# Optimization experiments

Measured on AMD Instinct MI355X. Metric: run time of the kernel, lower is better.

The kernel has to match this reference:

```python
import jax, jax.numpy as jnp
import numpy as np

N_NODES = 50000
N_EDGES = 800000
IN_F, EDGE_F, HID, HEADS, OUT_F = 128, 16, 32, 4, 128
NEG_SLOPE = 0.2


def edge_gat_layer(h, ef, src, dst, W, We, al, ar, ae, b, act):
    """One DGL-style EdgeGATConv layer.
    h: [N, Fin], ef: [E, Fe], W: [Fin, H*D], We: [Fe, H*D],
    al/ar/ae: [H, D], b: [H*D]. Returns [N, H*D].
    """
    N = h.shape[0]
    H, D = al.shape
    feat = (h @ W).reshape(N, H, D)                    # [N,H,D]
    fe = (ef @ We).reshape(-1, H, D)                   # [E,H,D]
    el = jnp.einsum('nhd,hd->nh', feat, al)            # [N,H]
    er = jnp.einsum('nhd,hd->nh', feat, ar)            # [N,H]
    ee = jnp.einsum('ehd,hd->eh', fe, ae)              # [E,H]
    e = jax.nn.leaky_relu(el[src] + er[dst] + ee, NEG_SLOPE)  # [E,H]
    # edge softmax over incoming edges of each dst node
    emax = jax.ops.segment_max(e, dst, num_segments=N)        # [N,H]
    ex = jnp.exp(e - emax[dst])                               # [E,H]
    esum = jax.ops.segment_sum(ex, dst, num_segments=N)       # [N,H]
    a = ex / esum[dst]                                        # [E,H]
    msg = feat[src] * a[:, :, None]                           # [E,H,D]
    rst = jax.ops.segment_sum(msg, dst, num_segments=N)       # [N,H,D]
    rst = rst + b.reshape(1, H, D)
    if act:
        rst = jax.nn.relu(rst)
    return rst.reshape(N, H * D)


def _glorot(k, shape):
    fan = shape[0]
    return jax.random.normal(k, shape, dtype=jnp.float32) / np.sqrt(fan)


def setup_inputs() -> dict:
    key = jax.random.key(0)
    ks = jax.random.split(key, 24)
    inp = {
        'h': jax.random.normal(ks[0], (N_NODES, IN_F), dtype=jnp.float32),
        'edge_feats': jax.random.normal(ks[1], (N_EDGES, EDGE_F), dtype=jnp.float32),
        'src': jax.random.randint(ks[2], (N_EDGES,), 0, N_NODES, dtype=jnp.int32),
        'dst': jax.random.randint(ks[3], (N_EDGES,), 0, N_NODES, dtype=jnp.int32),
    }
    # layer 0: IN_F -> HEADS*HID ; layer 1: HEADS*HID -> HEADS*HID ; layer 2: heads=1, OUT_F
    dims = [(IN_F, HEADS, HID), (HEADS * HID, HEADS, HID), (HEADS * HID, 1, OUT_F)]
    ki = 4
    for i, (fin, H, D) in enumerate(dims):
        inp[f'W{i}'] = _glorot(ks[ki], (fin, H * D)); ki += 1
        inp[f'We{i}'] = _glorot(ks[ki], (EDGE_F, H * D)); ki += 1
        inp[f'al{i}'] = _glorot(ks[ki], (H, D)); ki += 1
        inp[f'ar{i}'] = _glorot(ks[ki], (H, D)); ki += 1
        inp[f'ae{i}'] = _glorot(ks[ki], (H, D)); ki += 1
        inp[f'b{i}'] = jnp.zeros((H * D,), dtype=jnp.float32)
    return inp


def reference(h, edge_feats, src, dst,
              W0, We0, al0, ar0, ae0, b0,
              W1, We1, al1, ar1, ae1, b1,
              W2, We2, al2, ar2, ae2, b2):
    h = edge_gat_layer(h, edge_feats, src, dst, W0, We0, al0, ar0, ae0, b0, True)
    h = edge_gat_layer(h, edge_feats, src, dst, W1, We1, al1, ar1, ae1, b1, True)
    h = edge_gat_layer(h, edge_feats, src, dst, W2, We2, al2, ar2, ae2, b2, False)
    return h
```

## Files before the change

kernel.cpp:

```cpp
#include <hip/hip_runtime.h>
#include <hip/hip_fp16.h>
#include <cstdint>

#define NN 50000
#define NE 800000
static constexpr int HD = 128;
static constexpr int EF_DIM = 16;
static constexpr int SCAN_B = 256;
static constexpr int NPARTS = (NN + SCAN_B - 1) / SCAN_B;

typedef _Float16 f16x4 __attribute__((ext_vector_type(4)));
typedef float f32x4 __attribute__((ext_vector_type(4)));

struct RecP {
    int src;
    int e;
    f16x4 p0;
    f16x4 p1;
    _Float16 p2;
    _Float16 pad;
};
union Rec32 { RecP r; float4 v[2]; };

__global__ __launch_bounds__(256) void k_prep(const float* __restrict__ h,
        const float* __restrict__ We0, const float* __restrict__ ae0,
        const float* __restrict__ We1, const float* __restrict__ ae1,
        const float* __restrict__ We2, const float* __restrict__ ae2,
        const float* __restrict__ W0, const float* __restrict__ W1,
        const float* __restrict__ W2,
        int* __restrict__ cnt, float* __restrict__ M,
        _Float16* __restrict__ Wht, _Float16* __restrict__ Xh) {
    const int b = blockIdx.x, t = threadIdx.x;
    if (b < 196) {
        int i = b * 256 + t;
        if (i < NN) cnt[i] = 0;
        return;
    }
    if (b < 199) {
        int l = b - 196;
        const float* We = (l == 0) ? We0 : (l == 1) ? We1 : We2;
        const float* ae = (l == 0) ? ae0 : (l == 1) ? ae1 : ae2;
        int H = (l == 2) ? 1 : 4, D = (l == 2) ? 128 : 32;
        if (t < EF_DIM * H) {
            int f = t / H, hh = t % H;
            float s = 0.f;
            for (int d = 0; d < D; d++) s += We[f * HD + hh * D + d] * ae[hh * D + d];
            M[l * 64 + f * H + hh] = s;
        }
        return;
    }
    if (b < 391) {
        int i = (b - 199) * 256 + t;
        int l = i >> 14, rem = i & 16383;
        int n = rem >> 7, k = rem & 127;
        const float* W = (l == 0) ? W0 : (l == 1) ? W1 : W2;
        Wht[(size_t)l * 16384 + n * 128 + k] = (_Float16)W[k * 128 + n];
        return;
    }
    {
        int i = (b - 391) * 256 + t;
        if (i < NN * 32) {
            float4 v = ((const float4*)h)[i];
            f16x4 o = {(_Float16)v.x, (_Float16)v.y, (_Float16)v.z, (_Float16)v.w};
            ((f16x4*)Xh)[i] = o;
        }
    }
}


__global__ void k_pos(const int* __restrict__ dst, int* __restrict__ cnt,
                      int* __restrict__ pos_loc) {
    int e = blockIdx.x * blockDim.x + threadIdx.x;
    if (e < NE) pos_loc[e] = atomicAdd(&cnt[dst[e]], 1);
}

__global__ __launch_bounds__(SCAN_B) void k_part(const int* __restrict__ deg,
                                                 int* __restrict__ part) {
    __shared__ int s[SCAN_B];
    int t = threadIdx.x;
    int i = blockIdx.x * SCAN_B + t;
    s[t] = (i < NN) ? deg[i] : 0;
    __syncthreads();
    for (int off = SCAN_B / 2; off > 0; off >>= 1) {
        if (t < off) s[t] += s[t + off];
        __syncthreads();
    }
    if (t == 0) part[blockIdx.x] = s[0];
}

__global__ __launch_bounds__(SCAN_B) void k_scanpart(int* __restrict__ part) {
    __shared__ int s[SCAN_B];
    int t = threadIdx.x;
    int v = (t < NPARTS) ? part[t] : 0;
    s[t] = v;
    __syncthreads();
    for (int off = 1; off < SCAN_B; off <<= 1) {
        int u = (t >= off) ? s[t - off] : 0;
        __syncthreads();
        s[t] += u;
        __syncthreads();
    }
    if (t < NPARTS) part[t] = s[t] - v;
}

__global__ __launch_bounds__(SCAN_B) void k_rowptr(const int* __restrict__ deg,
                                                   const int* __restrict__ part,
                                                   int* __restrict__ row_ptr) {
    __shared__ int s[SCAN_B];
    int t = threadIdx.x;
    int i = blockIdx.x * SCAN_B + t;
    int v = (i < NN) ? deg[i] : 0;
    s[t] = v;
    __syncthreads();
    for (int off = 1; off < SCAN_B; off <<= 1) {
        int u = (t >= off) ? s[t - off] : 0;
        __syncthreads();
        s[t] += u;
        __syncthreads();
    }
    int excl = s[t] - v + part[blockIdx.x];
    if (i < NN) row_ptr[i] = excl;
    if (i == NN) row_ptr[NN] = NE;
}

__global__ __launch_bounds__(256) void k_place(const int* __restrict__ src,
                                               const int* __restrict__ dst,
                                               const int* __restrict__ pos_loc,
                                               const float* __restrict__ EFt,
                                               const float* __restrict__ M,
                                               const int* __restrict__ row_ptr,
                                               float4* __restrict__ rec) {
    __shared__ float sM[192];
    int t = threadIdx.x;
    if (t < 192) sM[t] = M[t];
    __syncthreads();
    int e = blockIdx.x * 256 + t;
    if (e >= NE) return;
    float ef[EF_DIM];
    const float4* efp = (const float4*)(EFt + (size_t)e * EF_DIM);
#pragma unroll
    for (int q = 0; q < 4; q++) {
        float4 v = efp[q];
        ef[4 * q] = v.x; ef[4 * q + 1] = v.y; ef[4 * q + 2] = v.z; ef[4 * q + 3] = v.w;
    }
    float o0[4] = {0.f, 0.f, 0.f, 0.f};
    float o1[4] = {0.f, 0.f, 0.f, 0.f};
    float o2 = 0.f;
#pragma unroll
    for (int f = 0; f < EF_DIM; f++) {
        float v = ef[f];
#pragma unroll
        for (int hh = 0; hh < 4; hh++) {
            o0[hh] += v * sM[f * 4 + hh];
            o1[hh] += v * sM[64 + f * 4 + hh];
        }
        o2 += v * sM[128 + f];
    }
    Rec32 u;
    u.r.src = src[e];
    u.r.e = e;
    u.r.p0 = f16x4{(_Float16)o0[0], (_Float16)o0[1], (_Float16)o0[2], (_Float16)o0[3]};
    u.r.p1 = f16x4{(_Float16)o1[0], (_Float16)o1[1], (_Float16)o1[2], (_Float16)o1[3]};
    u.r.p2 = (_Float16)o2;
    u.r.pad = (_Float16)0.f;
    int pos = row_ptr[dst[e]] + pos_loc[e];
    rec[(size_t)pos * 2] = u.v[0];
    rec[(size_t)pos * 2 + 1] = u.v[1];
}

__global__ __launch_bounds__(256) void k_segsort2(const int* __restrict__ row_ptr,
                                                  const float4* __restrict__ rec,
                                                  int* __restrict__ ssrc,
                                                  f16x4* __restrict__ ep0,
                                                  f16x4* __restrict__ ep1,
                                                  _Float16* __restrict__ ep2) {
    __shared__ Rec32 seg[4][128];
    const int wave = threadIdx.x >> 6;
    const int lane = threadIdx.x & 63;
    const int n = blockIdx.x * 4 + wave;
    const int start = row_ptr[n];
    const int len = row_ptr[n + 1] - start;
    const bool small = (len > 0 && len <= 128);
    if (small)
        for (int s = lane; s < len; s += 64) {
            seg[wave][s].v[0] = rec[(size_t)(start + s) * 2];
            seg[wave][s].v[1] = rec[(size_t)(start + s) * 2 + 1];
        }
    __syncthreads();
    if (small) {
        for (int s = lane; s < len; s += 64) {
            RecP me = seg[wave][s].r;
            int rank = 0;
            for (int j = 0; j < len; j++) {
                const RecP& o = seg[wave][j].r;
                rank += (o.src < me.src) || (o.src == me.src && o.e < me.e);
            }
            int w = start + rank;
            ssrc[w] = me.src;
            ep0[w] = me.p0;
            ep1[w] = me.p1;
            ep2[w] = me.p2;
        }
    } else if (len > 128) {
        for (int s = lane; s < len; s += 64) {
            Rec32 u;
            u.v[0] = rec[(size_t)(start + s) * 2];
            u.v[1] = rec[(size_t)(start + s) * 2 + 1];
            int w = start + s;
            ssrc[w] = u.r.src;
            ep0[w] = u.r.p0;
            ep1[w] = u.r.p1;
            ep2[w] = u.r.p2;
        }
    }
}


template <int H>
__global__ __launch_bounds__(256) void k_feat(const _Float16* __restrict__ Xh,
                                              const _Float16* __restrict__ Wht,
                                              const float* __restrict__ al,
                                              const float* __restrict__ ar,
                                              _Float16* __restrict__ Fh,
                                              float* __restrict__ el,
                                              float* __restrict__ er) {
    const int t = threadIdx.x;
    const int lane = t & 63;
    const int wv = t >> 6;
    const int l15 = lane & 15;
    const int kg = lane >> 4;
    const int nbase = blockIdx.x * 64;
    const int arow = nbase + wv * 16 + l15;
    const int rclamp = (arow < NN) ? arow : NN - 1;
    const int ksub = kg * 4;
    f16x4 a[8];
#pragma unroll
    for (int kb = 0; kb < 8; kb++)
        a[kb] = *(const f16x4*)(Xh + (size_t)rclamp * 128 + kb * 16 + ksub);

    const int r0 = nbase + wv * 16 + kg * 4;
    float slp[4][H], srp[4][H];
#pragma unroll
    for (int r = 0; r < 4; r++)
#pragma unroll
        for (int hh = 0; hh < H; hh++) { slp[r][hh] = 0.f; srp[r][hh] = 0.f; }

#pragma unroll
    for (int nt = 0; nt < 8; nt++) {
        f32x4 acc = {0.f, 0.f, 0.f, 0.f};
        const int nc = nt * 16 + l15;
        const _Float16* wp = Wht + (size_t)nc * 128;
#pragma unroll
        for (int kb = 0; kb < 8; kb++) {
            f16x4 bf = *(const f16x4*)(wp + kb * 16 + ksub);
            acc = __builtin_amdgcn_mfma_f32_16x16x16f16(a[kb], bf, acc, 0, 0, 0);
        }
        const float alv = al[nc], arv = ar[nc];
        constexpr int HSEL = 0;
        const int hsel = (H == 4) ? (nt >> 1) : HSEL;
#pragma unroll
        for (int r = 0; r < 4; r++) {
            int ro = r0 + r;
            if (ro < NN) Fh[(size_t)ro * 128 + nc] = (_Float16)acc[r];
            slp[r][hsel] += acc[r] * alv;
            srp[r][hsel] += acc[r] * arv;
        }
    }

#pragma unroll
    for (int m = 1; m < 16; m <<= 1)
#pragma unroll
        for (int r = 0; r < 4; r++)
#pragma unroll
            for (int hh = 0; hh < H; hh++) {
                slp[r][hh] += __shfl_xor(slp[r][hh], m);
                srp[r][hh] += __shfl_xor(srp[r][hh], m);
            }

    if (H == 4) {
        int r = l15 >> 2, hh2 = l15 & 3;
        float sv = 0.f, ev = 0.f;
#pragma unroll
        for (int rr = 0; rr < 4; rr++)
#pragma unroll
            for (int hc = 0; hc < H; hc++)
                if (rr == r && hc == hh2) { sv = slp[rr][hc]; ev = srp[rr][hc]; }
        int ro = r0 + r;
        if (ro < NN) { el[ro * 4 + hh2] = sv; er[ro * 4 + hh2] = ev; }
    } else {
        if (l15 < 4) {
            float sv = 0.f, ev = 0.f;
#pragma unroll
            for (int rr = 0; rr < 4; rr++)
                if (rr == l15) { sv = slp[rr][0]; ev = srp[rr][0]; }
            int ro = r0 + l15;
            if (ro < NN) { el[ro] = sv; er[ro] = ev; }
        }
    }
}

template <int H, int D, int OUT16>
__global__ __launch_bounds__(256) void k_node(const int* __restrict__ row_ptr,
                                              const int* __restrict__ ssrc,
                                              const _Float16* __restrict__ ep,
                                              const float* __restrict__ el,
                                              const float* __restrict__ er,
                                              const __half2* __restrict__ Fh,
                                              const float* __restrict__ bias,
                                              float* __restrict__ Rf,
                                              _Float16* __restrict__ Rh,
                                              int act) {
    __shared__ float wlds[4][256];
    const int wave = threadIdx.x >> 6;
    const int lane = threadIdx.x & 63;
    const int n = blockIdx.x * 4 + wave;
    const int start = row_ptr[n];
    const int end = row_ptr[n + 1];
    const int len = end - start;
    const int slots = len * H;
    const int c = 2 * lane;
    const int hcol = c / D;
    float2 b2 = make_float2(bias[c], bias[c + 1]);
    float2 a = make_float2(0.f, 0.f);

    if (len > 0) {
        constexpr int hsh = (H == 4) ? 2 : 0;
        const int hh = lane & (H - 1);
        const float er_j = er[n * H + hh];
        const _Float16* epb = ep + (size_t)start * H;
        float pmax = -3.0e38f, psum = 0.f;

        if (slots <= 256) {
            float* wp = wlds[wave];
            for (int jj = lane; jj < slots; jj += 64) {
                int i = start + (jj >> hsh);
                float x = el[ssrc[i] * H + hh] + er_j + (float)epb[jj];
                x = (x > 0.f) ? x : 0.2f * x;
                wp[jj] = x;
                pmax = fmaxf(pmax, x);
            }
            for (int m = H; m < 64; m <<= 1) pmax = fmaxf(pmax, __shfl_xor(pmax, m));
            for (int jj = lane; jj < slots; jj += 64) {
                float ex = __expf(wp[jj] - pmax);
                wp[jj] = ex;
                psum += ex;
            }
            for (int m = H; m < 64; m <<= 1) psum += __shfl_xor(psum, m);
            const float inv = 1.f / __shfl(psum, hcol);
#pragma unroll 4
            for (int i = start; i < end; i++) {
                float w = wp[(i - start) * H + hcol];
                float2 f2 = __half22float2(Fh[(size_t)ssrc[i] * 64 + lane]);
                a.x += f2.x * w;
                a.y += f2.y * w;
            }
            a.x *= inv;
            a.y *= inv;
        } else {
            for (int jj = lane; jj < slots; jj += 64) {
                int i = start + (jj >> hsh);
                float x = el[ssrc[i] * H + hh] + er_j + (float)epb[jj];
                x = (x > 0.f) ? x : 0.2f * x;
                pmax = fmaxf(pmax, x);
            }
            for (int m = H; m < 64; m <<= 1) pmax = fmaxf(pmax, __shfl_xor(pmax, m));
            for (int jj = lane; jj < slots; jj += 64) {
                int i = start + (jj >> hsh);
                float x = el[ssrc[i] * H + hh] + er_j + (float)epb[jj];
                x = (x > 0.f) ? x : 0.2f * x;
                psum += __expf(x - pmax);
            }
            for (int m = H; m < 64; m <<= 1) psum += __shfl_xor(psum, m);
            const float inv = 1.f / __shfl(psum, hcol);
            const float pm_c = __shfl(pmax, hcol);
            const float er_c = er[n * H + hcol];
            for (int i = start; i < end; i++) {
                int sn = ssrc[i];
                float x = el[sn * H + hcol] + er_c + (float)epb[(i - start) * H + hcol];
                x = (x > 0.f) ? x : 0.2f * x;
                float w = __expf(x - pm_c);
                float2 f2 = __half22float2(Fh[(size_t)sn * 64 + lane]);
                a.x += f2.x * w;
                a.y += f2.y * w;
            }
            a.x *= inv;
            a.y *= inv;
        }
    }

    float2 v = make_float2(a.x + b2.x, a.y + b2.y);
    if (act) { v.x = fmaxf(v.x, 0.f); v.y = fmaxf(v.y, 0.f); }
    if (OUT16)
        ((__half2*)Rh)[(size_t)n * 64 + lane] = __floats2half2_rn(v.x, v.y);
    else
        ((float2*)Rf)[(size_t)n * 64 + lane] = v;
}


extern "C" void kernel_launch(void* const* d_in, const int* in_sizes, int n_in,
                              void* d_out, int out_size, void* d_ws, size_t ws_size,
                              hipStream_t stream) {
    const float* h   = (const float*)d_in[0];
    const float* eft = (const float*)d_in[1];
    const int* src   = (const int*)d_in[2];
    const int* dst   = (const int*)d_in[3];
    auto P = [&](int i) { return (const float*)d_in[i]; };

    float* ws = (float*)d_ws;
    float4* rec    = (float4*)ws;
    _Float16* Fh   = (_Float16*)ws;
    float* el      = ws + 3200000;
    float* er      = ws + 3400000;
    _Float16* Xh   = (_Float16*)(ws + 6400000);
    _Float16* Wht  = (_Float16*)(ws + 9600000);
    _Float16* ep0s = Wht + 3 * 16384;
    _Float16* ep1s = ep0s + (size_t)NE * 4;
    _Float16* ep2s = ep1s + (size_t)NE * 4;
    int* ssrc      = (int*)(ep2s + NE);
    int* pos_loc   = ssrc + NE;
    float* M       = (float*)(pos_loc + NE);
    int* row_ptr   = (int*)(M + 192);
    int* cnt       = row_ptr + (NN + 1);
    int* part      = cnt + NN;
    float* out     = (float*)d_out;

    hipLaunchKernelGGL(k_prep, dim3(391 + (NN * 32 + 255) / 256), dim3(256), 0, stream,
                       h, P(5), P(8), P(11), P(14), P(17), P(20),
                       P(4), P(10), P(16), cnt, M, Wht, Xh);
    hipLaunchKernelGGL(k_pos, dim3((NE + 255) / 256), dim3(256), 0, stream,
                       dst, cnt, pos_loc);
    hipLaunchKernelGGL(k_part, dim3(NPARTS), dim3(SCAN_B), 0, stream, cnt, part);
    hipLaunchKernelGGL(k_scanpart, dim3(1), dim3(SCAN_B), 0, stream, part);
    hipLaunchKernelGGL(k_rowptr, dim3(NPARTS), dim3(SCAN_B), 0, stream,
                       cnt, part, row_ptr);
    hipLaunchKernelGGL(k_place, dim3((NE + 255) / 256), dim3(256), 0, stream,
                       src, dst, pos_loc, eft, M, row_ptr, rec);
    hipLaunchKernelGGL(k_segsort2, dim3(NN / 4), dim3(256), 0, stream,
                       row_ptr, rec, ssrc, (f16x4*)ep0s, (f16x4*)ep1s, ep2s);

    const int FG = (NN + 63) / 64;
    hipLaunchKernelGGL((k_feat<4>), dim3(FG), dim3(256), 0, stream,
                       Xh, Wht, P(6), P(7), Fh, el, er);
    hipLaunchKernelGGL((k_node<4, 32, 1>), dim3(NN / 4), dim3(256), 0, stream,
                       row_ptr, ssrc, ep0s, el, er, (const __half2*)Fh, P(9),
                       nullptr, Xh, 1);
    hipLaunchKernelGGL((k_feat<4>), dim3(FG), dim3(256), 0, stream,
                       Xh, Wht + 16384, P(12), P(13), Fh, el, er);
    hipLaunchKernelGGL((k_node<4, 32, 1>), dim3(NN / 4), dim3(256), 0, stream,
                       row_ptr, ssrc, ep1s, el, er, (const __half2*)Fh, P(15),
                       nullptr, Xh, 1);
    hipLaunchKernelGGL((k_feat<1>), dim3(FG), dim3(256), 0, stream,
                       Xh, Wht + 32768, P(18), P(19), Fh, el, er);
    hipLaunchKernelGGL((k_node<1, 128, 0>), dim3(NN / 4), dim3(256), 0, stream,
                       row_ptr, ssrc, ep2s, el, er, (const __half2*)Fh, P(21),
                       out, nullptr, 0);
}
```

Measured before the change: 367.6 us.

## Merge edge counting into prep and fuse layer-0 feature GEMM with edge placement

The edge-count atomics move into the prep kernel, and a small separate kernel now zeroes the counters first. The layer-0 feature GEMM is merged into the edge placement kernel as extra blocks, so the two independent pieces of work share one launch. To make that legal, Fh, el and er move to their own workspace region so they no longer alias the rec buffer. The aggregation loop unroll goes from 4 to 8. This removes kernel launches and lets independent work overlap, at the cost of a larger workspace and a mixed-block kernel whose register use is set by the heavier branch.

```diff
diff --git a/kernel.cpp b/kernel.cpp
--- a/kernel.cpp
+++ b/kernel.cpp
@@ -8,6 +8,8 @@
 static constexpr int EF_DIM = 16;
 static constexpr int SCAN_B = 256;
 static constexpr int NPARTS = (NN + SCAN_B - 1) / SCAN_B;
+static constexpr int EBLK = (NE + 255) / 256;
+static constexpr int FG = (NN + 63) / 64;
 
 typedef _Float16 f16x4 __attribute__((ext_vector_type(4)));
 typedef float f32x4 __attribute__((ext_vector_type(4)));
@@ -22,22 +24,159 @@
 };
 union Rec32 { RecP r; float4 v[2]; };
 
-__global__ __launch_bounds__(256) void k_prep(const float* __restrict__ h,
+
+template <int H>
+__device__ __forceinline__ void feat_body(int bid, const _Float16* __restrict__ Xh,
+                                          const _Float16* __restrict__ Wht,
+                                          const float* __restrict__ al,
+                                          const float* __restrict__ ar,
+                                          _Float16* __restrict__ Fh,
+                                          float* __restrict__ el,
+                                          float* __restrict__ er) {
+    const int t = threadIdx.x;
+    const int lane = t & 63;
+    const int wv = t >> 6;
+    const int l15 = lane & 15;
+    const int kg = lane >> 4;
+    const int nbase = bid * 64;
+    const int arow = nbase + wv * 16 + l15;
+    const int rclamp = (arow < NN) ? arow : NN - 1;
+    const int ksub = kg * 4;
+    f16x4 a[8];
+#pragma unroll
+    for (int kb = 0; kb < 8; kb++)
+        a[kb] = *(const f16x4*)(Xh + (size_t)rclamp * 128 + kb * 16 + ksub);
+
+    const int r0 = nbase + wv * 16 + kg * 4;
+    float slp[4][H], srp[4][H];
+#pragma unroll
+    for (int r = 0; r < 4; r++)
+#pragma unroll
+        for (int hh = 0; hh < H; hh++) { slp[r][hh] = 0.f; srp[r][hh] = 0.f; }
+
+#pragma unroll
+    for (int nt = 0; nt < 8; nt++) {
+        f32x4 acc = {0.f, 0.f, 0.f, 0.f};
+        const int nc = nt * 16 + l15;
+        const _Float16* wp = Wht + (size_t)nc * 128;
+#pragma unroll
+        for (int kb = 0; kb < 8; kb++) {
+            f16x4 bf = *(const f16x4*)(wp + kb * 16 + ksub);
+            acc = __builtin_amdgcn_mfma_f32_16x16x16f16(a[kb], bf, acc, 0, 0, 0);
+        }
+        const float alv = al[nc], arv = ar[nc];
+        const int hsel = (H == 4) ? (nt >> 1) : 0;
+#pragma unroll
+        for (int r = 0; r < 4; r++) {
+            int ro = r0 + r;
+            if (ro < NN) Fh[(size_t)ro * 128 + nc] = (_Float16)acc[r];
+            slp[r][hsel] += acc[r] * alv;
+            srp[r][hsel] += acc[r] * arv;
+        }
+    }
+
+#pragma unroll
+    for (int m = 1; m < 16; m <<= 1)
+#pragma unroll
+        for (int r = 0; r < 4; r++)
+#pragma unroll
+            for (int hh = 0; hh < H; hh++) {
+                slp[r][hh] += __shfl_xor(slp[r][hh], m);
+                srp[r][hh] += __shfl_xor(srp[r][hh], m);
+            }
+
+    if (H == 4) {
+        int r = l15 >> 2, hh2 = l15 & 3;
+        float sv = 0.f, ev = 0.f;
+#pragma unroll
+        for (int rr = 0; rr < 4; rr++)
+#pragma unroll
+            for (int hc = 0; hc < H; hc++)
+                if (rr == r && hc == hh2) { sv = slp[rr][hc]; ev = srp[rr][hc]; }
+        int ro = r0 + r;
+        if (ro < NN) { el[ro * 4 + hh2] = sv; er[ro * 4 + hh2] = ev; }
+    } else {
+        if (l15 < 4) {
+            float sv = 0.f, ev = 0.f;
+#pragma unroll
+            for (int rr = 0; rr < 4; rr++)
+                if (rr == l15) { sv = slp[rr][0]; ev = srp[rr][0]; }
+            int ro = r0 + l15;
+            if (ro < NN) { el[ro] = sv; er[ro] = ev; }
+        }
+    }
+}
+
+__device__ __forceinline__ void place_body(int bid, const int* __restrict__ src,
+                                           const int* __restrict__ dst,
+                                           const int* __restrict__ pos_loc,
+                                           const float* __restrict__ EFt,
+                                           const float* __restrict__ M,
+                                           const int* __restrict__ row_ptr,
+                                           float4* __restrict__ rec) {
+    __shared__ float sM[192];
+    int t = threadIdx.x;
+    if (t < 192) sM[t] = M[t];
+    __syncthreads();
+    int e = bid * 256 + t;
+    if (e >= NE) return;
+    float ef[EF_DIM];
+    const float4* efp = (const float4*)(EFt + (size_t)e * EF_DIM);
+#pragma unroll
+    for (int q = 0; q < 4; q++) {
+        float4 v = efp[q];
+        ef[4 * q] = v.x; ef[4 * q + 1] = v.y; ef[4 * q + 2] = v.z; ef[4 * q + 3] = v.w;
+    }
+    float o0[4] = {0.f, 0.f, 0.f, 0.f};
+    float o1[4] = {0.f, 0.f, 0.f, 0.f};
+    float o2 = 0.f;
+#pragma unroll
+    for (int f = 0; f < EF_DIM; f++) {
+        float v = ef[f];
+#pragma unroll
+        for (int hh = 0; hh < 4; hh++) {
+            o0[hh] += v * sM[f * 4 + hh];
+            o1[hh] += v * sM[64 + f * 4 + hh];
+        }
+        o2 += v * sM[128 + f];
+    }
+    Rec32 u;
+    u.r.src = src[e];
+    u.r.e = e;
+    u.r.p0 = f16x4{(_Float16)o0[0], (_Float16)o0[1], (_Float16)o0[2], (_Float16)o0[3]};
+    u.r.p1 = f16x4{(_Float16)o1[0], (_Float16)o1[1], (_Float16)o1[2], (_Float16)o1[3]};
+    u.r.p2 = (_Float16)o2;
+    u.r.pad = (_Float16)0.f;
+    int pos = row_ptr[dst[e]] + pos_loc[e];
+    rec[(size_t)pos * 2] = u.v[0];
+    rec[(size_t)pos * 2 + 1] = u.v[1];
+}
+
+
+__global__ void k_zero(int* __restrict__ cnt) {
+    int i = blockIdx.x * blockDim.x + threadIdx.x;
+    if (i < NN) cnt[i] = 0;
+}
+
+__global__ __launch_bounds__(256) void k_prep2(const float* __restrict__ h,
+        const int* __restrict__ dst,
         const float* __restrict__ We0, const float* __restrict__ ae0,
         const float* __restrict__ We1, const float* __restrict__ ae1,
         const float* __restrict__ We2, const float* __restrict__ ae2,
         const float* __restrict__ W0, const float* __restrict__ W1,
         const float* __restrict__ W2,
-        int* __restrict__ cnt, float* __restrict__ M,
+        int* __restrict__ cnt, int* __restrict__ pos_loc, float* __restrict__ M,
         _Float16* __restrict__ Wht, _Float16* __restrict__ Xh) {
-    const int b = blockIdx.x, t = threadIdx.x;
-    if (b < 196) {
-        int i = b * 256 + t;
-        if (i < NN) cnt[i] = 0;
+    int b = blockIdx.x;
+    const int t = threadIdx.x;
+    if (b < EBLK) {
+        int e = b * 256 + t;
+        if (e < NE) pos_loc[e] = atomicAdd(&cnt[dst[e]], 1);
         return;
     }
-    if (b < 199) {
-        int l = b - 196;
+    b -= EBLK;
+    if (b < 3) {
+        int l = b;
         const float* We = (l == 0) ? We0 : (l == 1) ? We1 : We2;
         const float* ae = (l == 0) ? ae0 : (l == 1) ? ae1 : ae2;
         int H = (l == 2) ? 1 : 4, D = (l == 2) ? 128 : 32;
@@ -49,8 +188,8 @@
         }
         return;
     }
-    if (b < 391) {
-        int i = (b - 199) * 256 + t;
+    if (b < 195) {
+        int i = (b - 3) * 256 + t;
         int l = i >> 14, rem = i & 16383;
         int n = rem >> 7, k = rem & 127;
         const float* W = (l == 0) ? W0 : (l == 1) ? W1 : W2;
@@ -58,20 +197,13 @@
         return;
     }
     {
-        int i = (b - 391) * 256 + t;
+        int i = (b - 195) * 256 + t;
         if (i < NN * 32) {
             float4 v = ((const float4*)h)[i];
             f16x4 o = {(_Float16)v.x, (_Float16)v.y, (_Float16)v.z, (_Float16)v.w};
             ((f16x4*)Xh)[i] = o;
         }
     }
-}
-
-
-__global__ void k_pos(const int* __restrict__ dst, int* __restrict__ cnt,
-                      int* __restrict__ pos_loc) {
-    int e = blockIdx.x * blockDim.x + threadIdx.x;
-    if (e < NE) pos_loc[e] = atomicAdd(&cnt[dst[e]], 1);
 }
 
 __global__ __launch_bounds__(SCAN_B) void k_part(const int* __restrict__ deg,
@@ -123,49 +255,18 @@
     if (i == NN) row_ptr[NN] = NE;
 }
 
-__global__ __launch_bounds__(256) void k_place(const int* __restrict__ src,
-                                               const int* __restrict__ dst,
-                                               const int* __restrict__ pos_loc,
-                                               const float* __restrict__ EFt,
-                                               const float* __restrict__ M,
-                                               const int* __restrict__ row_ptr,
-                                               float4* __restrict__ rec) {
-    __shared__ float sM[192];
-    int t = threadIdx.x;
-    if (t < 192) sM[t] = M[t];
-    __syncthreads();
-    int e = blockIdx.x * 256 + t;
-    if (e >= NE) return;
-    float ef[EF_DIM];
-    const float4* efp = (const float4*)(EFt + (size_t)e * EF_DIM);
-#pragma unroll
-    for (int q = 0; q < 4; q++) {
-        float4 v = efp[q];
-        ef[4 * q] = v.x; ef[4 * q + 1] = v.y; ef[4 * q + 2] = v.z; ef[4 * q + 3] = v.w;
-    }
-    float o0[4] = {0.f, 0.f, 0.f, 0.f};
-    float o1[4] = {0.f, 0.f, 0.f, 0.f};
-    float o2 = 0.f;
-#pragma unroll
-    for (int f = 0; f < EF_DIM; f++) {
-        float v = ef[f];
-#pragma unroll
-        for (int hh = 0; hh < 4; hh++) {
-            o0[hh] += v * sM[f * 4 + hh];
-            o1[hh] += v * sM[64 + f * 4 + hh];
-        }
-        o2 += v * sM[128 + f];
-    }
-    Rec32 u;
-    u.r.src = src[e];
-    u.r.e = e;
-    u.r.p0 = f16x4{(_Float16)o0[0], (_Float16)o0[1], (_Float16)o0[2], (_Float16)o0[3]};
-    u.r.p1 = f16x4{(_Float16)o1[0], (_Float16)o1[1], (_Float16)o1[2], (_Float16)o1[3]};
-    u.r.p2 = (_Float16)o2;
-    u.r.pad = (_Float16)0.f;
-    int pos = row_ptr[dst[e]] + pos_loc[e];
-    rec[(size_t)pos * 2] = u.v[0];
-    rec[(size_t)pos * 2 + 1] = u.v[1];
+__global__ __launch_bounds__(256) void k_place_feat(const int* __restrict__ src,
+        const int* __restrict__ dst, const int* __restrict__ pos_loc,
+        const float* __restrict__ EFt, const float* __restrict__ M,
+        const int* __restrict__ row_ptr, float4* __restrict__ rec,
+        const _Float16* __restrict__ Xh, const _Float16* __restrict__ Wht,
+        const float* __restrict__ al0, const float* __restrict__ ar0,
+        _Float16* __restrict__ Fh, float* __restrict__ el, float* __restrict__ er) {
+    int b = blockIdx.x;
+    if (b < EBLK)
+        place_body(b, src, dst, pos_loc, EFt, M, row_ptr, rec);
+    else
+        feat_body<4>(b - EBLK, Xh, Wht, al0, ar0, Fh, el, er);
 }
 
 __global__ __launch_bounds__(256) void k_segsort2(const int* __restrict__ row_ptr,
@@ -215,7 +316,6 @@
     }
 }
 
-
 template <int H>
 __global__ __launch_bounds__(256) void k_feat(const _Float16* __restrict__ Xh,
                                               const _Float16* __restrict__ Wht,
@@ -224,79 +324,7 @@
                                               _Float16* __restrict__ Fh,
                                               float* __restrict__ el,
                                               float* __restrict__ er) {
-    const int t = threadIdx.x;
-    const int lane = t & 63;
-    const int wv = t >> 6;
-    const int l15 = lane & 15;
-    const int kg = lane >> 4;
-    const int nbase = blockIdx.x * 64;
-    const int arow = nbase + wv * 16 + l15;
-    const int rclamp = (arow < NN) ? arow : NN - 1;
-    const int ksub = kg * 4;
-    f16x4 a[8];
-#pragma unroll
-    for (int kb = 0; kb < 8; kb++)
-        a[kb] = *(const f16x4*)(Xh + (size_t)rclamp * 128 + kb * 16 + ksub);
-
-    const int r0 = nbase + wv * 16 + kg * 4;
-    float slp[4][H], srp[4][H];
-#pragma unroll
-    for (int r = 0; r < 4; r++)
-#pragma unroll
-        for (int hh = 0; hh < H; hh++) { slp[r][hh] = 0.f; srp[r][hh] = 0.f; }
-
-#pragma unroll
-    for (int nt = 0; nt < 8; nt++) {
-        f32x4 acc = {0.f, 0.f, 0.f, 0.f};
-        const int nc = nt * 16 + l15;
-        const _Float16* wp = Wht + (size_t)nc * 128;
-#pragma unroll
-        for (int kb = 0; kb < 8; kb++) {
-            f16x4 bf = *(const f16x4*)(wp + kb * 16 + ksub);
-            acc = __builtin_amdgcn_mfma_f32_16x16x16f16(a[kb], bf, acc, 0, 0, 0);
-        }
-        const float alv = al[nc], arv = ar[nc];
-        constexpr int HSEL = 0;
-        const int hsel = (H == 4) ? (nt >> 1) : HSEL;
-#pragma unroll
-        for (int r = 0; r < 4; r++) {
-            int ro = r0 + r;
-            if (ro < NN) Fh[(size_t)ro * 128 + nc] = (_Float16)acc[r];
-            slp[r][hsel] += acc[r] * alv;
-            srp[r][hsel] += acc[r] * arv;
-        }
-    }
-
-#pragma unroll
-    for (int m = 1; m < 16; m <<= 1)
-#pragma unroll
-        for (int r = 0; r < 4; r++)
-#pragma unroll
-            for (int hh = 0; hh < H; hh++) {
-                slp[r][hh] += __shfl_xor(slp[r][hh], m);
-                srp[r][hh] += __shfl_xor(srp[r][hh], m);
-            }
-
-    if (H == 4) {
-        int r = l15 >> 2, hh2 = l15 & 3;
-        float sv = 0.f, ev = 0.f;
-#pragma unroll
-        for (int rr = 0; rr < 4; rr++)
-#pragma unroll
-            for (int hc = 0; hc < H; hc++)
-                if (rr == r && hc == hh2) { sv = slp[rr][hc]; ev = srp[rr][hc]; }
-        int ro = r0 + r;
-        if (ro < NN) { el[ro * 4 + hh2] = sv; er[ro * 4 + hh2] = ev; }
-    } else {
-        if (l15 < 4) {
-            float sv = 0.f, ev = 0.f;
-#pragma unroll
-            for (int rr = 0; rr < 4; rr++)
-                if (rr == l15) { sv = slp[rr][0]; ev = srp[rr][0]; }
-            int ro = r0 + l15;
-            if (ro < NN) { el[ro] = sv; er[ro] = ev; }
-        }
-    }
+    feat_body<H>(blockIdx.x, Xh, Wht, al, ar, Fh, el, er);
 }
 
 template <int H, int D, int OUT16>
@@ -347,7 +375,7 @@
             }
             for (int m = H; m < 64; m <<= 1) psum += __shfl_xor(psum, m);
             const float inv = 1.f / __shfl(psum, hcol);
-#pragma unroll 4
+#pragma unroll 8
             for (int i = start; i < end; i++) {
                 float w = wp[(i - start) * H + hcol];
                 float2 f2 = __half22float2(Fh[(size_t)ssrc[i] * 64 + lane]);
@@ -408,11 +436,8 @@
 
     float* ws = (float*)d_ws;
     float4* rec    = (float4*)ws;
-    _Float16* Fh   = (_Float16*)ws;
-    float* el      = ws + 3200000;
-    float* er      = ws + 3400000;
     _Float16* Xh   = (_Float16*)(ws + 6400000);
-    _Float16* Wht  = (_Float16*)(ws + 9600000);
+    _Float16* Wht  = Xh + (size_t)NN * 128;
     _Float16* ep0s = Wht + 3 * 16384;
     _Float16* ep1s = ep0s + (size_t)NE * 4;
     _Float16* ep2s = ep1s + (size_t)NE * 4;
@@ -422,25 +447,25 @@
     int* row_ptr   = (int*)(M + 192);
     int* cnt       = row_ptr + (NN + 1);
     int* part      = cnt + NN;
+    _Float16* Fh   = (_Float16*)(part + NPARTS + 64);
+    float* el      = (float*)(Fh + (size_t)NN * 128);
+    float* er      = el + (size_t)NN * 4;
     float* out     = (float*)d_out;
 
-    hipLaunchKernelGGL(k_prep, dim3(391 + (NN * 32 + 255) / 256), dim3(256), 0, stream,
-                       h, P(5), P(8), P(11), P(14), P(17), P(20),
-                       P(4), P(10), P(16), cnt, M, Wht, Xh);
-    hipLaunchKernelGGL(k_pos, dim3((NE + 255) / 256), dim3(256), 0, stream,
-                       dst, cnt, pos_loc);
+    hipLaunchKernelGGL(k_zero, dim3(NPARTS), dim3(256), 0, stream, cnt);
+    hipLaunchKernelGGL(k_prep2, dim3(EBLK + 195 + (NN * 32 + 255) / 256), dim3(256), 0,
+                       stream, h, dst, P(5), P(8), P(11), P(14), P(17), P(20),
+                       P(4), P(10), P(16), cnt, pos_loc, M, Wht, Xh);
     hipLaunchKernelGGL(k_part, dim3(NPARTS), dim3(SCAN_B), 0, stream, cnt, part);
     hipLaunchKernelGGL(k_scanpart, dim3(1), dim3(SCAN_B), 0, stream, part);
     hipLaunchKernelGGL(k_rowptr, dim3(NPARTS), dim3(SCAN_B), 0, stream,
                        cnt, part, row_ptr);
-    hipLaunchKernelGGL(k_place, dim3((NE + 255) / 256), dim3(256), 0, stream,
-                       src, dst, pos_loc, eft, M, row_ptr, rec);
+    hipLaunchKernelGGL(k_place_feat, dim3(EBLK + FG), dim3(256), 0, stream,
+                       src, dst, pos_loc, eft, M, row_ptr, rec,
+                       Xh, Wht, P(6), P(7), Fh, el, er);
     hipLaunchKernelGGL(k_segsort2, dim3(NN / 4), dim3(256), 0, stream,
                        row_ptr, rec, ssrc, (f16x4*)ep0s, (f16x4*)ep1s, ep2s);
 
-    const int FG = (NN + 63) / 64;
-    hipLaunchKernelGGL((k_feat<4>), dim3(FG), dim3(256), 0, stream,
-                       Xh, Wht, P(6), P(7), Fh, el, er);
     hipLaunchKernelGGL((k_node<4, 32, 1>), dim3(NN / 4), dim3(256), 0, stream,
                        row_ptr, ssrc, ep0s, el, er, (const __half2*)Fh, P(9),
                        nullptr, Xh, 1);
```

After: 366.3 us. About the same (-0.4%).
